# Performance work log

Hardware: AMD Instinct MI355X
Metric: run time of the kernel (lower is better)

## Reference

```python
import jax, jax.numpy as jnp
import numpy as np

N = 8192
D = 128
NUM_CLASSES = 16
EPS = 1e-8  # torch cosine_similarity eps


def setup_inputs() -> dict:
    key = jax.random.key(0)
    k1, k2 = jax.random.split(key)
    inp = jax.random.normal(k1, (N, D), dtype=jnp.float32)
    targets = jax.random.randint(k2, (N,), 0, NUM_CLASSES, dtype=jnp.int64)
    temperature = jnp.asarray(0.5, dtype=jnp.float32)
    return {"input": inp, "targets": targets, "temperature": temperature}


def reference(input, targets, temperature):
    # clamp temperature to [0.1, 1.0] as the module does in forward
    temp = jnp.clip(temperature, 0.1, 1.0)

    # cosine similarity matrix [N, N]
    norms = jnp.maximum(jnp.linalg.norm(input, axis=1, keepdims=True), EPS)
    xn = input / norms
    sim = jnp.matmul(xn, xn.T) / temp          # [N, N]
    E = jnp.exp(sim)                            # [N, N]

    same = targets[:, None] == targets[None, :]  # [N, N] bool
    diag = jnp.diagonal(E)                       # exp(s_ii)
    pos = jnp.sum(jnp.where(same, E, 0.0), axis=1) - diag   # same-class, excl self
    tot = jnp.sum(E, axis=1) - diag                          # pos + neg
    per_sample_loss = -jnp.log(pos / tot)                    # [N]

    # per-class aggregation (segment sums with static num_segments)
    counts = jax.ops.segment_sum(jnp.ones_like(per_sample_loss), targets,
                                 num_segments=NUM_CLASSES)
    sums = jax.ops.segment_sum(per_sample_loss, targets,
                               num_segments=NUM_CLASSES)
    safe_counts = jnp.maximum(counts, 1.0)
    class_mean = sums / safe_counts

    # class weights: (1/count) normalized over present classes
    inv = jnp.where(counts > 0, 1.0 / safe_counts, 0.0)
    weights = inv / jnp.sum(inv)

    # only classes with more than one sample contribute
    valid = counts > 1
    weighted = jnp.where(valid, class_mean * weights, 0.0)
    n_valid = jnp.sum(valid.astype(jnp.float32))
    loss = jnp.sum(weighted) / n_valid
    return loss
```

## Files before the change

### kernel.cpp

```cpp
#include <hip/hip_runtime.h>

#define N 8192
#define D 128
#define NCLS 16
#define SLOT 512
#define RSTRIDE 256

typedef unsigned short u16;
typedef __attribute__((ext_vector_type(8))) short v8s;
typedef __attribute__((ext_vector_type(16))) float f32x16;

static __device__ inline u16 f2bf(float f) {
  unsigned int u = __builtin_bit_cast(unsigned int, f);
  unsigned int r = u + 0x7fffu + ((u >> 16) & 1u);
  return (u16)(r >> 16);
}

__global__ __launch_bounds__(256) void k_norm(float* __restrict__ buf,
                                              const float* __restrict__ temp) {
  int wave = threadIdx.x >> 6;
  int lane = threadIdx.x & 63;
  int row = blockIdx.x * 4 + wave;
  const float* p = buf + (size_t)row * D + lane * 2;
  float x = p[0], y = p[1];
  float ss = x * x + y * y;
#pragma unroll
  for (int m = 32; m >= 1; m >>= 1) ss += __shfl_xor(ss, m);
  float t = fminf(fmaxf(temp[0], 0.1f), 1.0f);
  float sc = sqrtf(1.4426950408889634f / t);
  float inv = sc / fmaxf(sqrtf(ss), 1e-8f);
  unsigned int u0 = (unsigned int)f2bf(x * inv);
  unsigned int u1 = (unsigned int)f2bf(y * inv);
  reinterpret_cast<unsigned int*>(buf)[(size_t)row * 128 + lane] = u0 | (u1 << 16);
}

__global__ __launch_bounds__(256) void k_sim(float* __restrict__ buf,
                                             const int* __restrict__ tgt) {
  __shared__ __align__(16) char lds[2][32 * 256];

  const int tid = threadIdx.x;
  const int wave = tid >> 6;
  const int lane = tid & 63;
  const int l31 = lane & 31;
  const int h = lane >> 5;
  const int lm = l31 & 15;

  const u16* xnb = reinterpret_cast<const u16*>(buf);

  const int rowstrip = blockIdx.x >> 5;
  const int cq = blockIdx.x & 31;
  const int rwb = rowstrip * 128 + wave * 32;
  const int colblock = cq * 256;

  v8s afrag[8];
  {
    const u16* ap = xnb + (size_t)(rwb + l31) * RSTRIDE + h * 8;
#pragma unroll
    for (int kk = 0; kk < 8; ++kk)
      afrag[kk] = *reinterpret_cast<const v8s*>(ap + kk * 16);
  }

  int trow[16];
#pragma unroll
  for (int r = 0; r < 16; ++r)
    trow[r] = tgt[rwb + ((r & 3) + 8 * (r >> 2) + 4 * h)];

  int tcolv[8];
#pragma unroll
  for (int g = 0; g < 8; ++g) tcolv[g] = tgt[colblock + g * 32 + l31];

  float tot_acc[16], pos_acc[16];
#pragma unroll
  for (int r = 0; r < 16; ++r) { tot_acc[r] = 0.f; pos_acc[r] = 0.f; }

  auto stage = [&](int g, int bsel) {
    int rowbase = colblock + g * 32;
#pragma unroll
    for (int i = 0; i < 2; ++i) {
      int L = i * 256 + tid;
      int row = L >> 4;
      int s = (L & 15) ^ (row & 15);
      const char* src = reinterpret_cast<const char*>(buf) +
                        (size_t)(rowbase + row) * SLOT + s * 16;
      char* dst = &lds[bsel][(i * 256 + wave * 64) * 16];
      __builtin_amdgcn_global_load_lds(
          (const __attribute__((address_space(1))) void*)src,
          (__attribute__((address_space(3))) void*)dst, 16, 0, 0);
    }
  };

  stage(0, 0);
  __syncthreads();

  const int lbase = l31 * 256;

#pragma unroll
  for (int g = 0; g < 8; ++g) {
    int cur = g & 1;
    if (g + 1 < 8) stage(g + 1, cur ^ 1);

    int c0 = colblock + g * 32;
    int tcol = tcolv[g];

    f32x16 acc;
#pragma unroll
    for (int r = 0; r < 16; ++r) acc[r] = 0.f;
    const char* lb = lds[cur];
#pragma unroll
    for (int kk = 0; kk < 8; ++kk) {
      v8s bf = *reinterpret_cast<const v8s*>(lb + lbase + (((2 * kk + h) ^ lm) << 4));
      acc = __builtin_amdgcn_mfma_f32_32x32x16_bf16(afrag[kk], bf, acc, 0, 0, 0);
    }

    if (c0 != rwb) {
#pragma unroll
      for (int r = 0; r < 16; ++r) {
        float e = __builtin_amdgcn_exp2f(acc[r]);
        tot_acc[r] += e;
        pos_acc[r] += (tcol == trow[r]) ? e : 0.f;
      }
    } else {
#pragma unroll
      for (int r = 0; r < 16; ++r) {
        float e = __builtin_amdgcn_exp2f(acc[r]);
        if (l31 == ((r & 3) + 8 * (r >> 2) + 4 * h)) e = 0.f;
        tot_acc[r] += e;
        pos_acc[r] += (tcol == trow[r]) ? e : 0.f;
      }
    }
    __syncthreads();
  }

#pragma unroll
  for (int r = 0; r < 16; ++r) {
    float p = pos_acc[r], q = tot_acc[r];
#pragma unroll
    for (int m = 1; m <= 16; m <<= 1) {
      p += __shfl_xor(p, m);
      q += __shfl_xor(q, m);
    }
    if (l31 == 0) {
      int row = rwb + ((r & 3) + 8 * (r >> 2) + 4 * h);
      float* slot = reinterpret_cast<float*>(
          reinterpret_cast<char*>(buf) + (size_t)row * SLOT + 256);
      slot[cq] = p;
      slot[32 + cq] = q;
    }
  }
}

__global__ __launch_bounds__(128) void k_tail_a(float* __restrict__ buf,
                                                const int* __restrict__ tgt) {
  __shared__ float cs[NCLS], cc[NCLS];
  int tid = threadIdx.x;
  if (tid < NCLS) { cs[tid] = 0.f; cc[tid] = 0.f; }
  __syncthreads();
  int row = blockIdx.x * 128 + tid;
  const float4* s4 = reinterpret_cast<const float4*>(
      reinterpret_cast<const char*>(buf) + (size_t)row * SLOT + 256);
  float pos = 0.f, tot = 0.f;
#pragma unroll
  for (int i = 0; i < 8; ++i) {
    float4 a = s4[i], b = s4[8 + i];
    pos += a.x + a.y + a.z + a.w;
    tot += b.x + b.y + b.z + b.w;
  }
  float loss = logf(tot) - logf(pos);
  int c = tgt[row];
  atomicAdd(&cs[c], loss);
  atomicAdd(&cc[c], 1.0f);
  __syncthreads();
  if (tid < 2 * NCLS) {
    float* dst = reinterpret_cast<float*>(
        reinterpret_cast<char*>(buf) + (size_t)blockIdx.x * SLOT);
    dst[tid] = (tid < NCLS) ? cs[tid] : cc[tid - NCLS];
  }
}

__global__ __launch_bounds__(1024) void k_final(const float* __restrict__ buf,
                                                float* __restrict__ out) {
  __shared__ float cs[NCLS], cc[NCLS];
  int tid = threadIdx.x;
  if (tid < NCLS) { cs[tid] = 0.f; cc[tid] = 0.f; }
  __syncthreads();
  {
    int b = tid >> 4, c = tid & 15;
    const float* src = reinterpret_cast<const float*>(
        reinterpret_cast<const char*>(buf) + (size_t)b * SLOT);
    atomicAdd(&cs[c], src[c]);
    atomicAdd(&cc[c], src[NCLS + c]);
  }
  __syncthreads();
  if (tid < 64) {
    int c = tid;
    float s = 0.f, n = 0.f;
    if (c < NCLS) { s = cs[c]; n = cc[c]; }
    float safe = fmaxf(n, 1.0f);
    float mean = s / safe;
    float inv = (n > 0.5f) ? 1.0f / safe : 0.f;
    float valid = (n > 1.5f) ? 1.f : 0.f;
    float w = (n > 1.5f) ? mean * inv : 0.f;
    float sinv = inv, sw = w, sv = valid;
#pragma unroll
    for (int m = 1; m <= 32; m <<= 1) {
      sinv += __shfl_xor(sinv, m);
      sw += __shfl_xor(sw, m);
      sv += __shfl_xor(sv, m);
    }
    if (c == 0) out[0] = sw / sinv / sv;
  }
}

extern "C" void kernel_launch(void* const* d_in, const int* in_sizes, int n_in,
                              void* d_out, int out_size, void* d_ws, size_t ws_size,
                              hipStream_t stream) {
  float* buf = (float*)d_in[0];
  const int* tgt = (const int*)d_in[1];
  const float* temp = (const float*)d_in[2];
  float* out = (float*)d_out;
  (void)d_ws; (void)ws_size;

  k_norm<<<N / 4, 256, 0, stream>>>(buf, temp);
  k_sim<<<2048, 256, 0, stream>>>(buf, tgt);
  k_tail_a<<<64, 128, 0, stream>>>(buf, tgt);
  k_final<<<1, 1024, 0, stream>>>(buf, out);
}
```

Before: 112.8 us.

## Fuse loss tail and final reduction into sim kernel via last-block atomics

Removes the two tail kernels and folds their work into the similarity kernel. Per-row partial sums are now accumulated with global atomics, and a per-rowstrip counter lets the last finishing block compute per-class losses for its rows. A grid-wide counter then lets the final block compute the scalar loss. This saves two kernel launches and the pass that re-read the per-row slots, at the cost of atomic contention, extra fences and non-deterministic float summation order.

```diff
diff --git a/kernel.cpp b/kernel.cpp
--- a/kernel.cpp
+++ b/kernel.cpp
@@ -7,8 +7,14 @@
 #define RSTRIDE 256
 
 typedef unsigned short u16;
+typedef unsigned int u32;
 typedef __attribute__((ext_vector_type(8))) short v8s;
 typedef __attribute__((ext_vector_type(16))) float f32x16;
+
+#define WS_CLS_SUM 0
+#define WS_CLS_CNT 16
+#define WS_RS_CTR  32
+#define WS_GRID_CTR 96
 
 static __device__ inline u16 f2bf(float f) {
   unsigned int u = __builtin_bit_cast(unsigned int, f);
@@ -17,10 +23,12 @@
 }
 
 __global__ __launch_bounds__(256) void k_norm(float* __restrict__ buf,
-                                              const float* __restrict__ temp) {
+                                              const float* __restrict__ temp,
+                                              u32* __restrict__ ws) {
   int wave = threadIdx.x >> 6;
   int lane = threadIdx.x & 63;
   int row = blockIdx.x * 4 + wave;
+  if (blockIdx.x == 0 && threadIdx.x < 128) ws[threadIdx.x] = 0u;
   const float* p = buf + (size_t)row * D + lane * 2;
   float x = p[0], y = p[1];
   float ss = x * x + y * y;
@@ -32,11 +40,19 @@
   unsigned int u0 = (unsigned int)f2bf(x * inv);
   unsigned int u1 = (unsigned int)f2bf(y * inv);
   reinterpret_cast<unsigned int*>(buf)[(size_t)row * 128 + lane] = u0 | (u1 << 16);
+  if (lane == 0) {
+    float2 z; z.x = 0.f; z.y = 0.f;
+    *reinterpret_cast<float2*>(reinterpret_cast<char*>(buf) + (size_t)row * SLOT + 256) = z;
+  }
 }
 
 __global__ __launch_bounds__(256) void k_sim(float* __restrict__ buf,
-                                             const int* __restrict__ tgt) {
+                                             const int* __restrict__ tgt,
+                                             u32* __restrict__ ws,
+                                             float* __restrict__ out) {
   __shared__ __align__(16) char lds[2][32 * 256];
+  __shared__ float cls_s[NCLS], cls_c[NCLS];
+  __shared__ int s_last, s_fin;
 
   const int tid = threadIdx.x;
   const int wave = tid >> 6;
@@ -46,6 +62,7 @@
   const int lm = l31 & 15;
 
   const u16* xnb = reinterpret_cast<const u16*>(buf);
+  float* wsf = reinterpret_cast<float*>(ws);
 
   const int rowstrip = blockIdx.x >> 5;
   const int cq = blockIdx.x & 31;
@@ -143,71 +160,61 @@
       int row = rwb + ((r & 3) + 8 * (r >> 2) + 4 * h);
       float* slot = reinterpret_cast<float*>(
           reinterpret_cast<char*>(buf) + (size_t)row * SLOT + 256);
-      slot[cq] = p;
-      slot[32 + cq] = q;
-    }
-  }
-}
-
-__global__ __launch_bounds__(128) void k_tail_a(float* __restrict__ buf,
-                                                const int* __restrict__ tgt) {
-  __shared__ float cs[NCLS], cc[NCLS];
-  int tid = threadIdx.x;
-  if (tid < NCLS) { cs[tid] = 0.f; cc[tid] = 0.f; }
+      atomicAdd(&slot[0], p);
+      atomicAdd(&slot[1], q);
+    }
+  }
+
+  __threadfence();
   __syncthreads();
-  int row = blockIdx.x * 128 + tid;
-  const float4* s4 = reinterpret_cast<const float4*>(
-      reinterpret_cast<const char*>(buf) + (size_t)row * SLOT + 256);
-  float pos = 0.f, tot = 0.f;
-#pragma unroll
-  for (int i = 0; i < 8; ++i) {
-    float4 a = s4[i], b = s4[8 + i];
-    pos += a.x + a.y + a.z + a.w;
-    tot += b.x + b.y + b.z + b.w;
-  }
-  float loss = logf(tot) - logf(pos);
-  int c = tgt[row];
-  atomicAdd(&cs[c], loss);
-  atomicAdd(&cc[c], 1.0f);
+  if (tid == 0) s_last = (atomicAdd(&ws[WS_RS_CTR + rowstrip], 1u) == 31u);
   __syncthreads();
-  if (tid < 2 * NCLS) {
-    float* dst = reinterpret_cast<float*>(
-        reinterpret_cast<char*>(buf) + (size_t)blockIdx.x * SLOT);
-    dst[tid] = (tid < NCLS) ? cs[tid] : cc[tid - NCLS];
-  }
-}
-
-__global__ __launch_bounds__(1024) void k_final(const float* __restrict__ buf,
-                                                float* __restrict__ out) {
-  __shared__ float cs[NCLS], cc[NCLS];
-  int tid = threadIdx.x;
-  if (tid < NCLS) { cs[tid] = 0.f; cc[tid] = 0.f; }
-  __syncthreads();
-  {
-    int b = tid >> 4, c = tid & 15;
-    const float* src = reinterpret_cast<const float*>(
-        reinterpret_cast<const char*>(buf) + (size_t)b * SLOT);
-    atomicAdd(&cs[c], src[c]);
-    atomicAdd(&cc[c], src[NCLS + c]);
-  }
-  __syncthreads();
-  if (tid < 64) {
-    int c = tid;
-    float s = 0.f, n = 0.f;
-    if (c < NCLS) { s = cs[c]; n = cc[c]; }
-    float safe = fmaxf(n, 1.0f);
-    float mean = s / safe;
-    float inv = (n > 0.5f) ? 1.0f / safe : 0.f;
-    float valid = (n > 1.5f) ? 1.f : 0.f;
-    float w = (n > 1.5f) ? mean * inv : 0.f;
-    float sinv = inv, sw = w, sv = valid;
-#pragma unroll
-    for (int m = 1; m <= 32; m <<= 1) {
-      sinv += __shfl_xor(sinv, m);
-      sw += __shfl_xor(sw, m);
-      sv += __shfl_xor(sv, m);
-    }
-    if (c == 0) out[0] = sw / sinv / sv;
+  if (s_last) {
+    __threadfence();
+    if (tid < NCLS) { cls_s[tid] = 0.f; cls_c[tid] = 0.f; }
+    __syncthreads();
+    if (tid < 128) {
+      int row = rowstrip * 128 + tid;
+      volatile float* slot = reinterpret_cast<volatile float*>(
+          reinterpret_cast<char*>(buf) + (size_t)row * SLOT + 256);
+      float pos = slot[0], tot = slot[1];
+      float loss = __logf(tot) - __logf(pos);
+      int c = tgt[row];
+      atomicAdd(&cls_s[c], loss);
+      atomicAdd(&cls_c[c], 1.0f);
+    }
+    __syncthreads();
+    if (tid < NCLS) {
+      atomicAdd(&wsf[WS_CLS_SUM + tid], cls_s[tid]);
+      atomicAdd(&wsf[WS_CLS_CNT + tid], cls_c[tid]);
+    }
+    __threadfence();
+    __syncthreads();
+    if (tid == 0) s_fin = (atomicAdd(&ws[WS_GRID_CTR], 1u) == 63u);
+    __syncthreads();
+    if (s_fin && tid < 64) {
+      __threadfence();
+      int c = tid;
+      float s = 0.f, n = 0.f;
+      if (c < NCLS) {
+        volatile float* vf = wsf;
+        s = vf[WS_CLS_SUM + c];
+        n = vf[WS_CLS_CNT + c];
+      }
+      float safe = fmaxf(n, 1.0f);
+      float mean = s / safe;
+      float inv = (n > 0.5f) ? 1.0f / safe : 0.f;
+      float valid = (n > 1.5f) ? 1.f : 0.f;
+      float w = (n > 1.5f) ? mean * inv : 0.f;
+      float sinv = inv, sw = w, sv = valid;
+#pragma unroll
+      for (int m = 1; m <= 32; m <<= 1) {
+        sinv += __shfl_xor(sinv, m);
+        sw += __shfl_xor(sw, m);
+        sv += __shfl_xor(sv, m);
+      }
+      if (c == 0) out[0] = sw / sinv / sv;
+    }
   }
 }
 
@@ -218,10 +225,8 @@
   const int* tgt = (const int*)d_in[1];
   const float* temp = (const float*)d_in[2];
   float* out = (float*)d_out;
-  (void)d_ws; (void)ws_size;
-
-  k_norm<<<N / 4, 256, 0, stream>>>(buf, temp);
-  k_sim<<<2048, 256, 0, stream>>>(buf, tgt);
-  k_tail_a<<<64, 128, 0, stream>>>(buf, tgt);
-  k_final<<<1, 1024, 0, stream>>>(buf, out);
-}
+  u32* ws = (u32*)d_ws;
+
+  k_norm<<<N / 4, 256, 0, stream>>>(buf, temp, ws);
+  k_sim<<<2048, 256, 0, stream>>>(buf, tgt, ws, out);
+}
```

Measured after the change: 279.7 us. +147.9%, slower.
